# Optimization experiments

Measured on AMD Instinct MI355X. Metric: run time of the kernel, lower is better.

Reference implementation:

```python
import jax, jax.numpy as jnp
import numpy as np

NEG_INF = jnp.float32(-1e16)


def _gat_layer(x, W, b, graph):
    # x: [B,N,D_in], W: [D_in,D_out], b: [D_out], graph: [N,N]
    h = x @ W  # [B,N,D_out]
    s = jnp.einsum('bnd,bmd->bnm', h, h) * graph  # [B,N,N]
    s = jnp.where(s == 0.0, NEG_INF, s)  # masked_fill(scores==0, -1e16)
    a = jax.nn.softmax(s, axis=-1)
    return jnp.einsum('bnm,bmd->bnd', a, h) + b


def setup_inputs() -> dict:
    key = jax.random.key(0)
    ks = jax.random.split(key, 9)
    B, N, T, C = 2, 2048, 3, 16
    H, HID, OUT = 4, 16, 16
    flow_x = jax.random.normal(ks[0], (B, N, T, C), dtype=jnp.float32)
    graph = jax.random.randint(ks[1], (N, N), 0, 2).astype(jnp.float32)
    W1 = jax.random.normal(ks[2], (T, H, C, HID), dtype=jnp.float32)
    b1 = jax.random.normal(ks[3], (T, H, HID), dtype=jnp.float32)
    W2 = jax.random.normal(ks[4], (T, H * HID, OUT), dtype=jnp.float32)
    b2 = jax.random.normal(ks[5], (T, OUT), dtype=jnp.float32)
    W3 = jax.random.normal(ks[6], (T * OUT, OUT), dtype=jnp.float32)
    b3 = jax.random.normal(ks[7], (OUT,), dtype=jnp.float32)
    return {"flow_x": flow_x, "graph": graph, "W1": W1, "b1": b1,
            "W2": W2, "b2": b2, "W3": W3, "b3": b3}


def reference(flow_x, graph, W1, b1, W2, b2, W3, b3):
    B, N, T, C = flow_x.shape
    leaky = lambda v: jax.nn.leaky_relu(v, negative_slope=0.01)
    outs = []
    for t in range(T):  # static loop over distinct per-timestep subnets
        f = flow_x[:, :, t, :]  # [B,N,C]
        # all heads at once: h: [B,H,N,HID]
        h = jnp.einsum('bnc,hcd->bhnd', f, W1[t])
        s = jnp.einsum('bhnd,bhmd->bhnm', h, h) * graph  # [B,H,N,N]
        s = jnp.where(s == 0.0, NEG_INF, s)
        a = jax.nn.softmax(s, axis=-1)
        r = jnp.einsum('bhnm,bhmd->bhnd', a, h) + b1[t][None, :, None, :]
        # concat heads along feature dim (head-major order like torch.cat)
        r = r.transpose(0, 2, 1, 3).reshape(B, N, -1)  # [B,N,H*HID]
        r = leaky(r)
        r = leaky(_gat_layer(r, W2[t], b2[t], graph))  # [B,N,OUT]
        outs.append(r)
    hidden = jnp.concatenate(outs, axis=2)  # [B,N,T*OUT]
    out = _gat_layer(hidden, W3, b3, graph)  # [B,N,OUT]
    return out[:, :, None, :]  # [B,N,1,OUT]
```

## Files before the change

### kernel.cpp

```cpp
#include <hip/hip_runtime.h>
#include <stdint.h>

static constexpr int N = 2048;
static constexpr int B = 2;
static constexpr int T = 3;
static constexpr int H = 4;
static constexpr int D = 16;
static constexpr float NEG = -1e30f;
static constexpr float LOG2E = 1.4426950408889634f;

typedef float v2f __attribute__((ext_vector_type(2)));
typedef float v4f __attribute__((ext_vector_type(4)));

__device__ __forceinline__ v2f pk_fma(v2f a, v2f b, v2f c) {
    return __builtin_elementwise_fma(a, b, c);
}

__global__ void pack_mask(const float* __restrict__ g, unsigned long long* __restrict__ mb) {
    int idx = blockIdx.x * 256 + threadIdx.x;
    float v = g[idx];
    unsigned long long bal = __ballot(v != 0.0f);
    if ((threadIdx.x & 63) == 0) mb[idx >> 6] = bal;
}

__global__ void k_h1(const float* __restrict__ fx, const float* __restrict__ W1,
                     float* __restrict__ h1) {
    int id = blockIdx.x * 256 + threadIdx.x;
    int n = id & (N - 1);
    int head = id >> 11;
    int t = head >> 3;
    int b = (head >> 2) & 1;
    int h = head & 3;
    const float* f = fx + (((size_t)(b * N + n)) * T + t) * D;
    const float* w = W1 + ((t * H + h) * D) * (size_t)D;
    float fr[D];
    const float4* f4 = (const float4*)f;
#pragma unroll
    for (int k = 0; k < 4; ++k) {
        float4 v = f4[k];
        fr[4*k] = v.x; fr[4*k+1] = v.y; fr[4*k+2] = v.z; fr[4*k+3] = v.w;
    }
    float acc[D] = {};
#pragma unroll
    for (int c = 0; c < D; ++c)
#pragma unroll
        for (int d = 0; d < D; ++d) acc[d] = fmaf(fr[c], w[c*D+d], acc[d]);
    float* o = h1 + (size_t)id * D;
#pragma unroll
    for (int d = 0; d < D; ++d) o[d] = acc[d];
}

template<int KIN, int SHIFT>
__global__ void k_rowmm(const float* __restrict__ x, const float* __restrict__ Wbase,
                        float* __restrict__ y) {
    int id = blockIdx.x * 256 + threadIdx.x;
    int r = id >> 2, q = id & 3;
    const float* __restrict__ xr = x + (size_t)r * KIN;
    const float* __restrict__ w = Wbase + (size_t)(r >> SHIFT) * KIN * D + q * 4;
    float acc[4] = {};
    const float4* x4 = (const float4*)xr;
#pragma unroll
    for (int c4 = 0; c4 < KIN/4; ++c4) {
        float4 xv = x4[c4];
        float xs[4] = {xv.x, xv.y, xv.z, xv.w};
#pragma unroll
        for (int p = 0; p < 4; ++p) {
            int c = c4*4 + p;
#pragma unroll
            for (int d = 0; d < 4; ++d) acc[d] = fmaf(xs[p], w[c*D+d], acc[d]);
        }
    }
    float* o = y + (size_t)r * D + q * 4;
#pragma unroll
    for (int d = 0; d < 4; ++d) o[d] = acc[d];
}

__device__ __forceinline__ void attn_slice(
        const float* __restrict__ hh, const uint32_t* __restrict__ mrow,
        const v2f (&hi)[8], int j0, int jlen,
        float& m, float& l, v2f (&o)[8]) {
    for (int w = 0; w < jlen/32; ++w) {
        uint32_t mw = mrow[w];
        const float* __restrict__ tb = hh + (size_t)(j0 + w*32) * D;
#pragma unroll 4
        for (int u = 0; u < 32; ++u) {
            const v4f* h4 = (const v4f*)(tb + u*D);
            v4f A = h4[0], Bv = h4[1], C = h4[2], Dv = h4[3];
            v2f a0 = {0.f, 0.f}, a1 = {0.f, 0.f};
            a0 = pk_fma(hi[0], A.lo,  a0); a1 = pk_fma(hi[1], A.hi,  a1);
            a0 = pk_fma(hi[2], Bv.lo, a0); a1 = pk_fma(hi[3], Bv.hi, a1);
            a0 = pk_fma(hi[4], C.lo,  a0); a1 = pk_fma(hi[5], C.hi,  a1);
            a0 = pk_fma(hi[6], Dv.lo, a0); a1 = pk_fma(hi[7], Dv.hi, a1);
            float s = (a0.x + a0.y) + (a1.x + a1.y);
            float se = (mw & (1u << u)) ? s : NEG;
            if (se > m) {
                float cc = __builtin_amdgcn_exp2f(m - se);
                l *= cc;
                v2f c2 = {cc, cc};
#pragma unroll
                for (int p = 0; p < 8; ++p) o[p] *= c2;
                m = se;
            }
            float wg = __builtin_amdgcn_exp2f(se - m);
            l += wg;
            v2f w2 = {wg, wg};
            o[0] = pk_fma(w2, A.lo,  o[0]);
            o[1] = pk_fma(w2, A.hi,  o[1]);
            o[2] = pk_fma(w2, Bv.lo, o[2]);
            o[3] = pk_fma(w2, Bv.hi, o[3]);
            o[4] = pk_fma(w2, C.lo,  o[4]);
            o[5] = pk_fma(w2, C.hi,  o[5]);
            o[6] = pk_fma(w2, Dv.lo, o[6]);
            o[7] = pk_fma(w2, Dv.hi, o[7]);
        }
    }
}

__device__ __forceinline__ void load_hi(const float* __restrict__ hh, int row, v2f (&hi)[8]) {
    const v4f* r4 = (const v4f*)(hh + (size_t)row * D);
#pragma unroll
    for (int k = 0; k < 4; ++k) {
        v4f v = r4[k];
        hi[2*k]   = v.lo * LOG2E;
        hi[2*k+1] = v.hi * LOG2E;
    }
}

template<int SPLIT>
__device__ __forceinline__ bool block_merge(
        int lane, int wv, float m, float l, const v2f (&o)[8],
        float& M, float& L, float (&O)[D]) {
    __shared__ float sm[SPLIT][64];
    __shared__ float sl[SPLIT][64];
    __shared__ float so[SPLIT][64][D+1];
    sm[wv][lane] = m;
    sl[wv][lane] = l;
#pragma unroll
    for (int k = 0; k < 8; ++k) {
        so[wv][lane][2*k]   = o[k].x;
        so[wv][lane][2*k+1] = o[k].y;
    }
    __syncthreads();
    if (threadIdx.x >= 64) return false;
    int r = threadIdx.x;
    M = sm[0][r];
#pragma unroll
    for (int s = 1; s < SPLIT; ++s) M = fmaxf(M, sm[s][r]);
    L = 0.f;
#pragma unroll
    for (int k = 0; k < D; ++k) O[k] = 0.f;
#pragma unroll
    for (int s = 0; s < SPLIT; ++s) {
        float cc = __builtin_amdgcn_exp2f(sm[s][r] - M);
        L = fmaf(cc, sl[s][r], L);
#pragma unroll
        for (int k = 0; k < D; ++k) O[k] = fmaf(cc, so[s][r][k], O[k]);
    }
    return true;
}

template<int SPLIT>
__global__ __launch_bounds__(64*SPLIT) void attn1(
        const float* __restrict__ hsrc, const uint32_t* __restrict__ mask,
        const float* __restrict__ bias, float* __restrict__ out) {
    constexpr int JLEN = N / SPLIT;
    const int lane = threadIdx.x & 63;
    const int wv = threadIdx.x >> 6;
    const int row = blockIdx.x * 64 + lane;
    const int head = blockIdx.y;
    const float* __restrict__ hh = hsrc + (size_t)head * N * D;

    v2f hi[8];
    load_hi(hh, row, hi);
    const int j0 = __builtin_amdgcn_readfirstlane(wv * JLEN);
    const uint32_t* __restrict__ mrow = mask + (size_t)row * (N/32) + (j0 >> 5);
    float m = NEG, l = 0.f;
    v2f o[8];
#pragma unroll
    for (int p = 0; p < 8; ++p) o[p] = (v2f){0.f, 0.f};
    attn_slice(hh, mrow, hi, j0, JLEN, m, l, o);

    float M, L, O[D];
    if (block_merge<SPLIT>(lane, wv, m, l, o, M, L, O)) {
        int t = head >> 3, b = (head >> 2) & 1, hd = head & 3;
        const float* bb = bias + (t * H + hd) * D;
        int rr = blockIdx.x * 64 + threadIdx.x;
        float* orow = out + ((size_t)(t * B + b) * N + rr) * (H * D) + hd * D;
        float inv = 1.0f / L;
#pragma unroll
        for (int k = 0; k < D; ++k) {
            float v = fmaf(O[k], inv, bb[k]);
            orow[k] = (v > 0.f) ? v : 0.01f * v;
        }
    }
}

template<int SPLIT, int JS>
__global__ __launch_bounds__(64*SPLIT) void attn_p(
        const float* __restrict__ hsrc, const uint32_t* __restrict__ mask,
        float* __restrict__ pm, float* __restrict__ pl, float* __restrict__ po) {
    constexpr int JLEN = N / (SPLIT * JS);
    static_assert(JLEN >= 32, "mask-word floor");
    const int lane = threadIdx.x & 63;
    const int wv = threadIdx.x >> 6;
    const int row = blockIdx.x * 64 + lane;
    const int head = blockIdx.y;
    const int js = blockIdx.z;
    const float* __restrict__ hh = hsrc + (size_t)head * N * D;

    v2f hi[8];
    load_hi(hh, row, hi);
    const int j0 = __builtin_amdgcn_readfirstlane((js * SPLIT + wv) * JLEN);
    const uint32_t* __restrict__ mrow = mask + (size_t)row * (N/32) + (j0 >> 5);
    float m = NEG, l = 0.f;
    v2f o[8];
#pragma unroll
    for (int p = 0; p < 8; ++p) o[p] = (v2f){0.f, 0.f};
    attn_slice(hh, mrow, hi, j0, JLEN, m, l, o);

    float M, L, O[D];
    if (block_merge<SPLIT>(lane, wv, m, l, o, M, L, O)) {
        int rr = blockIdx.x * 64 + threadIdx.x;
        size_t pidx = ((size_t)head * N + rr) * JS + js;
        pm[pidx] = M;
        pl[pidx] = L;
#pragma unroll
        for (int k = 0; k < D; ++k) po[pidx * D + k] = O[k];
    }
}

template<int JS, int LAYER, bool LEAKY>
__global__ void k_merge(const float* __restrict__ pm, const float* __restrict__ pl,
                        const float* __restrict__ po, const float* __restrict__ bias,
                        float* __restrict__ out) {
    int id = blockIdx.x * 256 + threadIdx.x;
    int row = id & (N - 1);
    int head = id >> 11;
    size_t base = (size_t)id * JS;
    float M = pm[base];
#pragma unroll
    for (int s = 1; s < JS; ++s) M = fmaxf(M, pm[base + s]);
    float L = 0.f, O[D] = {};
#pragma unroll
    for (int s = 0; s < JS; ++s) {
        float cc = __builtin_amdgcn_exp2f(pm[base + s] - M);
        L = fmaf(cc, pl[base + s], L);
        const float* pp = po + (base + s) * D;
#pragma unroll
        for (int k = 0; k < D; ++k) O[k] = fmaf(cc, pp[k], O[k]);
    }
    const float* bb; float* orow;
    if constexpr (LAYER == 2) {
        int t = head >> 1, b = head & 1;
        bb = bias + t * D;
        orow = out + ((size_t)b * N + row) * (T * D) + t * D;
    } else {
        bb = bias;
        orow = out + ((size_t)head * N + row) * D;
    }
    float inv = 1.0f / L;
#pragma unroll
    for (int k = 0; k < D; ++k) {
        float v = fmaf(O[k], inv, bb[k]);
        if (LEAKY) v = (v > 0.f) ? v : 0.01f * v;
        orow[k] = v;
    }
}

extern "C" void kernel_launch(void* const* d_in, const int* in_sizes, int n_in,
                              void* d_out, int out_size, void* d_ws, size_t ws_size,
                              hipStream_t stream) {
    const float* fx    = (const float*)d_in[0];
    const float* graph = (const float*)d_in[1];
    const float* W1    = (const float*)d_in[2];
    const float* b1    = (const float*)d_in[3];
    const float* W2    = (const float*)d_in[4];
    const float* b2    = (const float*)d_in[5];
    const float* W3    = (const float*)d_in[6];
    const float* b3    = (const float*)d_in[7];
    float* out = (float*)d_out;

    char* ws = (char*)d_ws;
    unsigned long long* mask64 = (unsigned long long*)ws;
    float* h1     = (float*)(ws + (size_t)(N*(size_t)N/8));
    float* x2     = h1 + (size_t)T*B*H*N*D;
    float* h2     = x2 + (size_t)T*B*N*H*D;
    float* hidden = h2 + (size_t)T*B*N*D;
    float* h3     = hidden + (size_t)B*N*T*D;

    constexpr size_t PMAX = (size_t)T*B*N*4;
    float* pm = h1;
    float* pl = h1 + PMAX;
    float* po = h1 + 2*PMAX;

    pack_mask<<<N*N/256, 256, 0, stream>>>(graph, mask64);
    k_h1<<<T*B*H*N/256, 256, 0, stream>>>(fx, W1, h1);

    attn1<8><<<dim3(N/64, T*B*H), 512, 0, stream>>>(h1, (const uint32_t*)mask64, b1, x2);
    k_rowmm<H*D,12><<<T*B*N*4/256, 256, 0, stream>>>(x2, W2, h2);

    attn_p<8,4><<<dim3(N/64, T*B, 4), 512, 0, stream>>>(h2, (const uint32_t*)mask64, pm, pl, po);
    k_merge<4,2,true><<<T*B*N/256, 256, 0, stream>>>(pm, pl, po, b2, hidden);

    k_rowmm<T*D,20><<<B*N*4/256, 256, 0, stream>>>(hidden, W3, h3);

    attn_p<8,8><<<dim3(N/64, B, 8), 512, 0, stream>>>(h3, (const uint32_t*)mask64, pm, pl, po);
    k_merge<8,3,false><<<B*N/256, 256, 0, stream>>>(pm, pl, po, b3, out);
}
```

Baseline: 292.4 us.

## Fuse prep kernels, split layer-1 attention over keys, use lazy wave-uniform rescale

Merges mask packing and the first projection into one launch. Replaces the single-pass layer-1 attention with a key-split partial attention plus merge, when the workspace is large enough, to gain more parallelism. Changes the online softmax so it rescales only when any lane's score exceeds the running max by more than 64 in log2 units, which avoids divergent per-element rescale branches but lets unnormalised weights grow up to 2^64. The lazy threshold risks numerical overflow, and the extra partial buffers add memory traffic.

Result: no change. 292.9 us (+0.2%).

```diff
diff --git a/kernel.cpp b/kernel.cpp
--- a/kernel.cpp
+++ b/kernel.cpp
@@ -12,20 +12,17 @@
 typedef float v2f __attribute__((ext_vector_type(2)));
 typedef float v4f __attribute__((ext_vector_type(4)));
 
-__device__ __forceinline__ v2f pk_fma(v2f a, v2f b, v2f c) {
-    return __builtin_elementwise_fma(a, b, c);
-}
-
-__global__ void pack_mask(const float* __restrict__ g, unsigned long long* __restrict__ mb) {
-    int idx = blockIdx.x * 256 + threadIdx.x;
-    float v = g[idx];
-    unsigned long long bal = __ballot(v != 0.0f);
-    if ((threadIdx.x & 63) == 0) mb[idx >> 6] = bal;
-}
-
-__global__ void k_h1(const float* __restrict__ fx, const float* __restrict__ W1,
-                     float* __restrict__ h1) {
-    int id = blockIdx.x * 256 + threadIdx.x;
+__global__ void k_prep(const float* __restrict__ g, unsigned long long* __restrict__ mb,
+                       const float* __restrict__ fx, const float* __restrict__ W1,
+                       float* __restrict__ h1) {
+    if (blockIdx.x < (unsigned)(N * N / 256)) {
+        int idx = blockIdx.x * 256 + threadIdx.x;
+        float v = g[idx];
+        unsigned long long bal = __ballot(v != 0.0f);
+        if ((threadIdx.x & 63) == 0) mb[idx >> 6] = bal;
+        return;
+    }
+    int id = (blockIdx.x - N * N / 256) * 256 + threadIdx.x;
     int n = id & (N - 1);
     int head = id >> 11;
     int t = head >> 3;
@@ -87,31 +84,36 @@
             const v4f* h4 = (const v4f*)(tb + u*D);
             v4f A = h4[0], Bv = h4[1], C = h4[2], Dv = h4[3];
             v2f a0 = {0.f, 0.f}, a1 = {0.f, 0.f};
-            a0 = pk_fma(hi[0], A.lo,  a0); a1 = pk_fma(hi[1], A.hi,  a1);
-            a0 = pk_fma(hi[2], Bv.lo, a0); a1 = pk_fma(hi[3], Bv.hi, a1);
-            a0 = pk_fma(hi[4], C.lo,  a0); a1 = pk_fma(hi[5], C.hi,  a1);
-            a0 = pk_fma(hi[6], Dv.lo, a0); a1 = pk_fma(hi[7], Dv.hi, a1);
+            a0 = __builtin_elementwise_fma(hi[0], A.lo,  a0);
+            a1 = __builtin_elementwise_fma(hi[1], A.hi,  a1);
+            a0 = __builtin_elementwise_fma(hi[2], Bv.lo, a0);
+            a1 = __builtin_elementwise_fma(hi[3], Bv.hi, a1);
+            a0 = __builtin_elementwise_fma(hi[4], C.lo,  a0);
+            a1 = __builtin_elementwise_fma(hi[5], C.hi,  a1);
+            a0 = __builtin_elementwise_fma(hi[6], Dv.lo, a0);
+            a1 = __builtin_elementwise_fma(hi[7], Dv.hi, a1);
             float s = (a0.x + a0.y) + (a1.x + a1.y);
             float se = (mw & (1u << u)) ? s : NEG;
-            if (se > m) {
-                float cc = __builtin_amdgcn_exp2f(m - se);
+            if (__any(se - m > 64.f)) {
+                float mn = fmaxf(m, se);
+                float cc = __builtin_amdgcn_exp2f(m - mn);
                 l *= cc;
                 v2f c2 = {cc, cc};
 #pragma unroll
                 for (int p = 0; p < 8; ++p) o[p] *= c2;
-                m = se;
+                m = mn;
             }
             float wg = __builtin_amdgcn_exp2f(se - m);
             l += wg;
             v2f w2 = {wg, wg};
-            o[0] = pk_fma(w2, A.lo,  o[0]);
-            o[1] = pk_fma(w2, A.hi,  o[1]);
-            o[2] = pk_fma(w2, Bv.lo, o[2]);
-            o[3] = pk_fma(w2, Bv.hi, o[3]);
-            o[4] = pk_fma(w2, C.lo,  o[4]);
-            o[5] = pk_fma(w2, C.hi,  o[5]);
-            o[6] = pk_fma(w2, Dv.lo, o[6]);
-            o[7] = pk_fma(w2, Dv.hi, o[7]);
+            o[0] = __builtin_elementwise_fma(w2, A.lo,  o[0]);
+            o[1] = __builtin_elementwise_fma(w2, A.hi,  o[1]);
+            o[2] = __builtin_elementwise_fma(w2, Bv.lo, o[2]);
+            o[3] = __builtin_elementwise_fma(w2, Bv.hi, o[3]);
+            o[4] = __builtin_elementwise_fma(w2, C.lo,  o[4]);
+            o[5] = __builtin_elementwise_fma(w2, C.hi,  o[5]);
+            o[6] = __builtin_elementwise_fma(w2, Dv.lo, o[6]);
+            o[7] = __builtin_elementwise_fma(w2, Dv.hi, o[7]);
         }
     }
 }
@@ -250,7 +252,11 @@
         for (int k = 0; k < D; ++k) O[k] = fmaf(cc, pp[k], O[k]);
     }
     const float* bb; float* orow;
-    if constexpr (LAYER == 2) {
+    if constexpr (LAYER == 1) {
+        int t = head >> 3, b = (head >> 2) & 1, hd = head & 3;
+        bb = bias + (t * H + hd) * D;
+        orow = out + ((size_t)(t * B + b) * N + row) * (H * D) + hd * D;
+    } else if constexpr (LAYER == 2) {
         int t = head >> 1, b = head & 1;
         bb = bias + t * D;
         orow = out + ((size_t)b * N + row) * (T * D) + t * D;
@@ -287,23 +293,34 @@
     float* h2     = x2 + (size_t)T*B*N*H*D;
     float* hidden = h2 + (size_t)T*B*N*D;
     float* h3     = hidden + (size_t)B*N*T*D;
-
-    constexpr size_t PMAX = (size_t)T*B*N*4;
-    float* pm = h1;
-    float* pl = h1 + PMAX;
-    float* po = h1 + 2*PMAX;
-
-    pack_mask<<<N*N/256, 256, 0, stream>>>(graph, mask64);
-    k_h1<<<T*B*H*N/256, 256, 0, stream>>>(fx, W1, h1);
-
-    attn1<8><<<dim3(N/64, T*B*H), 512, 0, stream>>>(h1, (const uint32_t*)mask64, b1, x2);
-    k_rowmm<H*D,12><<<T*B*N*4/256, 256, 0, stream>>>(x2, W2, h2);
-
-    attn_p<8,4><<<dim3(N/64, T*B, 4), 512, 0, stream>>>(h2, (const uint32_t*)mask64, pm, pl, po);
-    k_merge<4,2,true><<<T*B*N/256, 256, 0, stream>>>(pm, pl, po, b2, hidden);
-
-    k_rowmm<T*D,20><<<B*N*4/256, 256, 0, stream>>>(hidden, W3, h3);
-
-    attn_p<8,8><<<dim3(N/64, B, 8), 512, 0, stream>>>(h3, (const uint32_t*)mask64, pm, pl, po);
-    k_merge<8,3,false><<<B*N/256, 256, 0, stream>>>(pm, pl, po, b3, out);
-}
+    float* tail   = h3 + (size_t)B*N*D;
+
+    constexpr size_t P1 = (size_t)T*B*H*N*2;
+    size_t need = ((char*)(tail + P1*2 + P1*D) - ws);
+    bool big = ws_size >= need;
+
+    k_prep<<<N*N/256 + T*B*H*N/256, 256, 0, stream>>>(graph, mask64, fx, W1, h1);
+
+    if (big) {
+        float* pm = tail, *pl = tail + P1, *po = tail + 2*P1;
+        attn_p<8,2><<<dim3(N/64, T*B*H, 2), 512, 0, stream>>>(h1, (const uint32_t*)mask64, pm, pl, po);
+        k_merge<2,1,true><<<T*B*H*N/256, 256, 0, stream>>>(pm, pl, po, b1, x2);
+        k_rowmm<H*D,12><<<T*B*N*4/256, 256, 0, stream>>>(x2, W2, h2);
+        attn_p<8,4><<<dim3(N/64, T*B, 4), 512, 0, stream>>>(h2, (const uint32_t*)mask64, pm, pl, po);
+        k_merge<4,2,true><<<T*B*N/256, 256, 0, stream>>>(pm, pl, po, b2, hidden);
+        k_rowmm<T*D,20><<<B*N*4/256, 256, 0, stream>>>(hidden, W3, h3);
+        attn_p<8,8><<<dim3(N/64, B, 8), 512, 0, stream>>>(h3, (const uint32_t*)mask64, pm, pl, po);
+        k_merge<8,3,false><<<B*N/256, 256, 0, stream>>>(pm, pl, po, b3, out);
+    } else {
+        float* fpm = h1;
+        float* fpl = h1 + (size_t)T*B*N*4;
+        float* fpo = h1 + 2*(size_t)T*B*N*4;
+        attn1<8><<<dim3(N/64, T*B*H), 512, 0, stream>>>(h1, (const uint32_t*)mask64, b1, x2);
+        k_rowmm<H*D,12><<<T*B*N*4/256, 256, 0, stream>>>(x2, W2, h2);
+        attn_p<8,4><<<dim3(N/64, T*B, 4), 512, 0, stream>>>(h2, (const uint32_t*)mask64, fpm, fpl, fpo);
+        k_merge<4,2,true><<<T*B*N/256, 256, 0, stream>>>(fpm, fpl, fpo, b2, hidden);
+        k_rowmm<T*D,20><<<B*N*4/256, 256, 0, stream>>>(hidden, W3, h3);
+        attn_p<8,8><<<dim3(N/64, B, 8), 512, 0, stream>>>(h3, (const uint32_t*)mask64, fpm, fpl, fpo);
+        k_merge<8,3,false><<<B*N/256, 256, 0, stream>>>(fpm, fpl, fpo, b3, out);
+    }
+}
```
